# Performance work log

Hardware: AMD Instinct MI355X
Metric: run time of the kernel (lower is better)

The kernel has to match this reference:

```python
import jax, jax.numpy as jnp
import numpy as np

TEMPERATURE = 0.5  # NT-Xent temperature (SimCLR default in SACLR)
NEG_INF = -1e9


def ntxent(zi, zj, temperature=TEMPERATURE):
    """SimCLR NT-Xent between two views zi, zj of shape [B, D]."""
    B = zi.shape[0]
    z = jnp.concatenate([zi, zj], axis=0)                      # [2B, D]
    z = z / (jnp.linalg.norm(z, axis=1, keepdims=True) + 1e-8)  # cosine sim
    sim = (z @ z.T) / temperature                              # [2B, 2B]
    n = 2 * B
    sim = jnp.where(jnp.eye(n, dtype=bool), NEG_INF, sim)      # mask self
    labels = jnp.concatenate([jnp.arange(B) + B, jnp.arange(B)])
    logp = jax.nn.log_softmax(sim, axis=1)
    return -jnp.mean(logp[jnp.arange(n), labels])


def setup_inputs() -> dict:
    key = jax.random.key(0)
    k1, k2, k3 = jax.random.split(key, 3)
    B, D, W, H, CA = 512, 256, 14, 14, 8
    return {
        "global_feature": jax.random.normal(k1, (B, D), dtype=jnp.float32),
        "att": jax.random.uniform(k2, (B, CA, W, H), dtype=jnp.float32),
        "outputs": jax.random.normal(k3, (B, D, W, H), dtype=jnp.float32),
    }


def reference(global_feature, att, outputs):
    # attention = sum over attention-map channel, shape [B, W, H]
    attention = jnp.sum(att, axis=1)
    B, D, W, H = outputs.shape
    P = W * H
    # Flatten spatial positions in the same (i over W, j over H) row-major order
    # as the original nested python loops.
    local_feats = jnp.transpose(outputs, (2, 3, 0, 1)).reshape(P, B, D)   # [P, B, D]
    local_atts = jnp.transpose(attention, (1, 2, 0)).reshape(P, B)        # [P, B]

    # Faithful quirk of the original: global_feature is re-softmaxed at every
    # spatial position (it is reassigned inside the loop), so carry it in a scan.
    def step(g, xs):
        lf, la = xs
        g = jax.nn.softmax(g, axis=1)          # repeated softmax on global
        lf = jax.nn.softmax(lf, axis=1)        # softmax on local feature
        l = ntxent(lf, g) * jnp.mean(la) / P   # weighted NT-Xent term
        return g, l

    _, losses = jax.lax.scan(step, global_feature, (local_feats, local_atts))
    return jnp.sum(losses)
```

## Files before the change

### kernel.cpp

```cpp
#include <hip/hip_runtime.h>

#define B_   512
#define D_   256
#define P_   196
#define N2B  1024

typedef __attribute__((ext_vector_type(8))) short short8;
typedef __attribute__((ext_vector_type(4))) float f32x4;
typedef unsigned int u32;

#define LDSP(x) ((__attribute__((address_space(3))) u32*)(x))
#define GLBP(x) ((const __attribute__((address_space(1))) u32*)(x))

__device__ unsigned short g_Z[(size_t)P_ * N2B * D_];
__device__ float g_rowps[(size_t)P_ * 8 * N2B];
__device__ float g_pp2[P_ * 4];
__device__ float g_mApart[32 * P_];
__device__ float g_partials[P_];

static __device__ const unsigned char TROW36[36] = {
  0,0,0,0,0,0,0,0, 1,1,1,1,1,1,1, 2,2,2,2,2,2, 3,3,3,3,3, 4,4,4,4, 5,5,5, 6,6, 7};
static __device__ const unsigned char TCOL36[36] = {
  0,1,2,3,4,5,6,7, 1,2,3,4,5,6,7, 2,3,4,5,6,7, 3,4,5,6,7, 4,5,6,7, 5,6,7, 6,7, 7};

static __device__ inline unsigned short f2bf(float f) {
    union { float f; unsigned int u; } v; v.f = f;
    unsigned int u = v.u;
    return (unsigned short)((u + 0x7fffu + ((u >> 16) & 1u)) >> 16);
}
static __device__ inline float bf2f(unsigned short h) {
    union { unsigned int u; float f; } v; v.u = ((unsigned int)h) << 16;
    return v.f;
}
static __device__ inline float wave_sum(float v) {
    for (int off = 32; off > 0; off >>= 1) v += __shfl_xor(v, off, 64);
    return v;
}

__global__ __launch_bounds__(256) void gchain_kernel(const float* __restrict__ gf) {
    int wv = threadIdx.x >> 6, lane = threadIdx.x & 63;
    int b = blockIdx.x * 4 + wv;
    float4 g = ((const float4*)(gf + (size_t)b * D_))[lane];
    for (int p = 0; p < P_; ++p) {
        float e0 = __expf(g.x), e1 = __expf(g.y), e2 = __expf(g.z), e3 = __expf(g.w);
        float s1 = e0 + e1 + e2 + e3;
        float s2 = e0 * e0 + e1 * e1 + e2 * e2 + e3 * e3;
#pragma unroll
        for (int off = 32; off > 0; off >>= 1) {
            s1 += __shfl_xor(s1, off, 64);
            s2 += __shfl_xor(s2, off, 64);
        }
        float isq = rsqrtf(s2);
        ushort4 o;
        o.x = f2bf(e0 * isq); o.y = f2bf(e1 * isq); o.z = f2bf(e2 * isq); o.w = f2bf(e3 * isq);
        ((ushort4*)(g_Z + ((size_t)p * N2B + B_ + b) * D_))[lane] = o;
        float inv = 1.0f / s1;
        g.x = e0 * inv; g.y = e1 * inv; g.z = e2 * inv; g.w = e3 * inv;
    }
}

__global__ __launch_bounds__(1024) void lf_kernel(const float* __restrict__ outs) {
    __shared__ unsigned short vt[256 * 202];
    __shared__ float ss[256];
    int b = blockIdx.x, t = threadIdx.x;
    const float4* src4 = (const float4*)(outs + (size_t)b * (D_ * P_));
    for (int idx = t; idx < 12544; idx += 1024) {
        int d = idx / 49, c = idx - d * 49;
        float4 v = src4[idx];
        unsigned short* dst = vt + d * 202 + c * 4;
        ushort2 a, bb;
        a.x = f2bf(v.x); a.y = f2bf(v.y); bb.x = f2bf(v.z); bb.y = f2bf(v.w);
        *(ushort2*)dst = a; *(ushort2*)(dst + 2) = bb;
    }
    __syncthreads();
    {
        int p = t >> 2; if (p > 195) p = 195;
        int s = t & 3;
        float r = 0.0f;
        for (int dd = 0; dd < 64; ++dd) {
            float v = bf2f(vt[(s * 64 + dd) * 202 + p]);
            r += __expf(2.0f * v);
        }
        r += __shfl_xor(r, 1, 64);
        r += __shfl_xor(r, 2, 64);
        if (s == 0) ss[p] = rsqrtf(r);
    }
    __syncthreads();
    {
        int d = t & 255, q = t >> 8;
        for (int pi = 0; pi < 49; ++pi) {
            int p = q * 49 + pi;
            float v = bf2f(vt[d * 202 + p]);
            g_Z[((size_t)p * N2B + b) * D_ + d] = f2bf(__expf(v) * ss[p]);
        }
    }
}

__global__ __launch_bounds__(256) void meanA_kernel(const float* __restrict__ att) {
    int bk = blockIdx.x, t = threadIdx.x;
    if (t < P_) {
        float acc = 0.0f;
        const float* base = att + (size_t)bk * 128 * P_ + t;
        for (int r = 0; r < 128; ++r) acc += base[(size_t)r * P_];
        g_mApart[bk * P_ + t] = acc;
    }
}

__global__ __launch_bounds__(256, 3) void sim_kernel() {
    __shared__ __align__(16) unsigned short As[128 * 64];
    __shared__ __align__(16) unsigned short Bs[128 * 64];
    __shared__ float combuf[512];
    __shared__ float ppred[4];

    int lin0 = blockIdx.x;
    int xcd = lin0 & 7, slot = lin0 >> 3;
    int lin = xcd * 882 + slot;
    int p = lin / 36;
    int t36 = lin - p * 36;
    int trow = TROW36[t36], tcol = TCOL36[t36];

    int tid = threadIdx.x;
    int wv = tid >> 6, lane = tid & 63;
    int wr = wv >> 1, wc = wv & 1;
    int lr = lane & 15;
    int lk16 = (lane >> 4) * 16;

    const char* zb = (const char*)g_Z + (size_t)p * ((size_t)N2B * D_ * 2);
    const char* gA = zb + (size_t)trow * (128 * 512);
    const char* gB = zb + (size_t)tcol * (128 * 512);
    int lsub = (lane >> 3) * 512 + (lane & 7) * 16;

    f32x4 acc[4][4];
#pragma unroll
    for (int i = 0; i < 4; ++i)
#pragma unroll
        for (int j = 0; j < 4; ++j)
            acc[i][j] = (f32x4){0.0f, 0.0f, 0.0f, 0.0f};

    for (int ko = 0; ko < 4; ++ko) {
#pragma unroll
        for (int it = 0; it < 4; ++it) {
            int s = it * 4 + wv;
            int go = s * 4096 + ko * 128 + lsub;
            __builtin_amdgcn_global_load_lds(GLBP(gA + go), LDSP((char*)As + s * 1024), 16, 0, 0);
            __builtin_amdgcn_global_load_lds(GLBP(gB + go), LDSP((char*)Bs + s * 1024), 16, 0, 0);
        }
        __syncthreads();
#pragma unroll
        for (int ks = 0; ks < 2; ++ks) {
            short8 a[4], b[4];
#pragma unroll
            for (int i = 0; i < 4; ++i) {
                a[i] = *(const short8*)((const char*)As + (wr * 64 + i * 16 + lr) * 128 + ks * 64 + lk16);
                b[i] = *(const short8*)((const char*)Bs + (wc * 64 + i * 16 + lr) * 128 + ks * 64 + lk16);
            }
#pragma unroll
            for (int i = 0; i < 4; ++i)
#pragma unroll
                for (int j = 0; j < 4; ++j)
                    acc[i][j] = __builtin_amdgcn_mfma_f32_16x16x32_bf16(a[i], b[j], acc[i][j], 0, 0, 0);
        }
        __syncthreads();
    }

    bool DIAG = (trow == tcol);
    bool PART = (trow < 4) && (tcol == trow + 4);
    int r4 = (lane >> 4) * 4;
    float psum[4][4];
    float pcs[4] = {0.0f, 0.0f, 0.0f, 0.0f};
    float pp = 0.0f;
#pragma unroll
    for (int i = 0; i < 4; ++i)
#pragma unroll
        for (int r = 0; r < 4; ++r) psum[i][r] = 0.0f;

#pragma unroll
    for (int i = 0; i < 4; ++i) {
#pragma unroll
        for (int j = 0; j < 4; ++j) {
#pragma unroll
            for (int r = 0; r < 4; ++r) {
                float sv = 2.0f * acc[i][j][r];
                float e = __expf(sv);
                int lrow = wr * 64 + i * 16 + r4 + r;
                int lcol = wc * 64 + j * 16 + lr;
                bool ond = (lrow == lcol);
                if (DIAG && ond) e = 0.0f;
                psum[i][r] += e;
                pcs[j] += e;
                if (PART && ond) pp += sv;
            }
        }
    }

    float* rowbuf = combuf;
    float* colbuf = combuf + 256;
#pragma unroll
    for (int i = 0; i < 4; ++i)
#pragma unroll
        for (int r = 0; r < 4; ++r) {
            float ps = psum[i][r];
            ps += __shfl_xor(ps, 1, 64);
            ps += __shfl_xor(ps, 2, 64);
            ps += __shfl_xor(ps, 4, 64);
            ps += __shfl_xor(ps, 8, 64);
            if (lr == 0) rowbuf[wc * 128 + wr * 64 + i * 16 + r4 + r] = ps;
        }
#pragma unroll
    for (int j = 0; j < 4; ++j) {
        float pc = pcs[j];
        pc += __shfl_xor(pc, 16, 64);
        pc += __shfl_xor(pc, 32, 64);
        if (lane < 16) colbuf[wr * 128 + wc * 64 + j * 16 + lane] = pc;
    }
    float pw = PART ? wave_sum(pp) : 0.0f;
    if (lane == 0) ppred[wv] = pw;
    __syncthreads();

    if (tid < 128) {
        float v = rowbuf[tid] + rowbuf[128 + tid];
        g_rowps[((size_t)p * 8 + tcol) * N2B + trow * 128 + tid] = v;
    } else if (!DIAG) {
        int x = tid - 128;
        float v = colbuf[x] + colbuf[128 + x];
        g_rowps[((size_t)p * 8 + trow) * N2B + tcol * 128 + x] = v;
    }
    if (PART && tid == 0)
        g_pp2[p * 4 + trow] = 2.0f * (ppred[0] + ppred[1] + ppred[2] + ppred[3]);
}

__global__ __launch_bounds__(256) void rowreduce_kernel() {
    int p = blockIdx.x, t = threadIdx.x;
    const float* base = g_rowps + (size_t)p * 8 * N2B;
    float s = 0.0f;
    for (int r = t; r < N2B; r += 256) {
        float S = 0.0f;
#pragma unroll
        for (int k = 0; k < 8; ++k) S += base[(size_t)k * N2B + r];
        s += __logf(S);
    }
    s = wave_sum(s);
    __shared__ float red[4];
    int wv = t >> 6, lane = t & 63;
    if (lane == 0) red[wv] = s;
    __syncthreads();
    if (t == 0) {
        float tot = red[0] + red[1] + red[2] + red[3];
        float pp = g_pp2[p * 4 + 0] + g_pp2[p * 4 + 1] + g_pp2[p * 4 + 2] + g_pp2[p * 4 + 3];
        float ma = 0.0f;
        for (int k = 0; k < 32; ++k) ma += g_mApart[k * P_ + p];
        g_partials[p] = (tot - pp) * (ma * (1.0f / B_));
    }
}

__global__ __launch_bounds__(256) void final_kernel(float* __restrict__ out) {
    int t = threadIdx.x;
    float s = (t < P_) ? g_partials[t] : 0.0f;
    s = wave_sum(s);
    __shared__ float red[4];
    int wv = t >> 6, lane = t & 63;
    if (lane == 0) red[wv] = s;
    __syncthreads();
    if (t == 0) out[0] = (red[0] + red[1] + red[2] + red[3]) * (1.0f / ((float)N2B * (float)P_));
}

extern "C" void kernel_launch(void* const* d_in, const int* in_sizes, int n_in,
                              void* d_out, int out_size, void* d_ws, size_t ws_size,
                              hipStream_t stream) {
    const float* gf   = (const float*)d_in[0];
    const float* att  = (const float*)d_in[1];
    const float* outs = (const float*)d_in[2];
    float* out = (float*)d_out;

    hipLaunchKernelGGL(gchain_kernel, dim3(B_ / 4), dim3(256), 0, stream, gf);
    hipLaunchKernelGGL(lf_kernel, dim3(B_), dim3(1024), 0, stream, outs);
    hipLaunchKernelGGL(meanA_kernel, dim3(32), dim3(256), 0, stream, att);
    hipLaunchKernelGGL(sim_kernel, dim3(P_ * 36), dim3(256), 0, stream);
    hipLaunchKernelGGL(rowreduce_kernel, dim3(P_), dim3(256), 0, stream);
    hipLaunchKernelGGL(final_kernel, dim3(1), dim3(256), 0, stream, out);
}
```

Before: 372.6 us.

## Fuse prep kernels, pre-scale embeddings for exp2, swizzle LDS, specialize epilogue

Merges the global-chain, local-feature and attention-mean kernels into one heterogeneous prep launch, with the attention mean split over more slices. Folds the 1/temperature and log2(e) factors into the bf16 normalized embeddings so the epilogue can use exp2 directly. Adds an XOR swizzle to the LDS tile layout to reduce bank conflicts on the MFMA operand reads, and splits the epilogue into diagonal, positive-pair and plain variants so masking and column sums run only where needed. It also raises the launch-bounds occupancy hint. Scaling before bf16 rounding slightly changes numerics, and the fused prep kernel mixes 1024-thread blocks with very different per-block work.

```diff
diff --git a/kernel.cpp b/kernel.cpp
--- a/kernel.cpp
+++ b/kernel.cpp
@@ -5,6 +5,9 @@
 #define P_   196
 #define N2B  1024
 
+#define CSCALE 1.69864364f
+#define LN2    0.69314718f
+
 typedef __attribute__((ext_vector_type(8))) short short8;
 typedef __attribute__((ext_vector_type(4))) float f32x4;
 typedef unsigned int u32;
@@ -15,7 +18,7 @@
 __device__ unsigned short g_Z[(size_t)P_ * N2B * D_];
 __device__ float g_rowps[(size_t)P_ * 8 * N2B];
 __device__ float g_pp2[P_ * 4];
-__device__ float g_mApart[32 * P_];
+__device__ float g_mApart[128 * P_];
 __device__ float g_partials[P_];
 
 static __device__ const unsigned char TROW36[36] = {
@@ -37,76 +40,103 @@
     return v;
 }
 
-__global__ __launch_bounds__(256) void gchain_kernel(const float* __restrict__ gf) {
-    int wv = threadIdx.x >> 6, lane = threadIdx.x & 63;
-    int b = blockIdx.x * 4 + wv;
-    float4 g = ((const float4*)(gf + (size_t)b * D_))[lane];
-    for (int p = 0; p < P_; ++p) {
-        float e0 = __expf(g.x), e1 = __expf(g.y), e2 = __expf(g.z), e3 = __expf(g.w);
-        float s1 = e0 + e1 + e2 + e3;
-        float s2 = e0 * e0 + e1 * e1 + e2 * e2 + e3 * e3;
-#pragma unroll
-        for (int off = 32; off > 0; off >>= 1) {
-            s1 += __shfl_xor(s1, off, 64);
-            s2 += __shfl_xor(s2, off, 64);
-        }
-        float isq = rsqrtf(s2);
-        ushort4 o;
-        o.x = f2bf(e0 * isq); o.y = f2bf(e1 * isq); o.z = f2bf(e2 * isq); o.w = f2bf(e3 * isq);
-        ((ushort4*)(g_Z + ((size_t)p * N2B + B_ + b) * D_))[lane] = o;
-        float inv = 1.0f / s1;
-        g.x = e0 * inv; g.y = e1 * inv; g.z = e2 * inv; g.w = e3 * inv;
-    }
-}
-
-__global__ __launch_bounds__(1024) void lf_kernel(const float* __restrict__ outs) {
+__global__ __launch_bounds__(1024) void prep_kernel(const float* __restrict__ gf,
+                                                    const float* __restrict__ att,
+                                                    const float* __restrict__ outs) {
     __shared__ unsigned short vt[256 * 202];
     __shared__ float ss[256];
-    int b = blockIdx.x, t = threadIdx.x;
-    const float4* src4 = (const float4*)(outs + (size_t)b * (D_ * P_));
-    for (int idx = t; idx < 12544; idx += 1024) {
-        int d = idx / 49, c = idx - d * 49;
-        float4 v = src4[idx];
-        unsigned short* dst = vt + d * 202 + c * 4;
-        ushort2 a, bb;
-        a.x = f2bf(v.x); a.y = f2bf(v.y); bb.x = f2bf(v.z); bb.y = f2bf(v.w);
-        *(ushort2*)dst = a; *(ushort2*)(dst + 2) = bb;
-    }
-    __syncthreads();
-    {
-        int p = t >> 2; if (p > 195) p = 195;
-        int s = t & 3;
-        float r = 0.0f;
-        for (int dd = 0; dd < 64; ++dd) {
-            float v = bf2f(vt[(s * 64 + dd) * 202 + p]);
-            r += __expf(2.0f * v);
-        }
-        r += __shfl_xor(r, 1, 64);
-        r += __shfl_xor(r, 2, 64);
-        if (s == 0) ss[p] = rsqrtf(r);
-    }
-    __syncthreads();
-    {
-        int d = t & 255, q = t >> 8;
-        for (int pi = 0; pi < 49; ++pi) {
-            int p = q * 49 + pi;
-            float v = bf2f(vt[d * 202 + p]);
-            g_Z[((size_t)p * N2B + b) * D_ + d] = f2bf(__expf(v) * ss[p]);
-        }
-    }
-}
-
-__global__ __launch_bounds__(256) void meanA_kernel(const float* __restrict__ att) {
-    int bk = blockIdx.x, t = threadIdx.x;
-    if (t < P_) {
-        float acc = 0.0f;
-        const float* base = att + (size_t)bk * 128 * P_ + t;
-        for (int r = 0; r < 128; ++r) acc += base[(size_t)r * P_];
-        g_mApart[bk * P_ + t] = acc;
-    }
-}
-
-__global__ __launch_bounds__(256, 3) void sim_kernel() {
+    int blk = blockIdx.x, t = threadIdx.x;
+
+    if (blk < 32) {
+        int wv = t >> 6, lane = t & 63;
+        int b = blk * 16 + wv;
+        float4 g = ((const float4*)(gf + (size_t)b * D_))[lane];
+        for (int p = 0; p < P_; ++p) {
+            float e0 = __expf(g.x), e1 = __expf(g.y), e2 = __expf(g.z), e3 = __expf(g.w);
+            float s1 = e0 + e1 + e2 + e3;
+            float s2 = e0 * e0 + e1 * e1 + e2 * e2 + e3 * e3;
+#pragma unroll
+            for (int off = 32; off > 0; off >>= 1) {
+                s1 += __shfl_xor(s1, off, 64);
+                s2 += __shfl_xor(s2, off, 64);
+            }
+            float isq = rsqrtf(s2) * CSCALE;
+            ushort4 o;
+            o.x = f2bf(e0 * isq); o.y = f2bf(e1 * isq); o.z = f2bf(e2 * isq); o.w = f2bf(e3 * isq);
+            ((ushort4*)(g_Z + ((size_t)p * N2B + B_ + b) * D_))[lane] = o;
+            float inv = 1.0f / s1;
+            g.x = e0 * inv; g.y = e1 * inv; g.z = e2 * inv; g.w = e3 * inv;
+        }
+    } else if (blk < 64) {
+        int bk = blk - 32;
+        int sl = t >> 8, p = t & 255;
+        if (p < P_) {
+            float acc = 0.0f;
+            const float* base = att + ((size_t)bk * 128 + sl * 32) * P_ + p;
+            for (int r = 0; r < 32; ++r) acc += base[(size_t)r * P_];
+            g_mApart[(bk * 4 + sl) * P_ + p] = acc;
+        }
+    } else {
+        int b = blk - 64;
+        const float4* src4 = (const float4*)(outs + (size_t)b * (D_ * P_));
+        for (int idx = t; idx < 12544; idx += 1024) {
+            int d = idx / 49, c = idx - d * 49;
+            float4 v = src4[idx];
+            unsigned short* dst = vt + d * 202 + c * 4;
+            ushort2 a, bb;
+            a.x = f2bf(v.x); a.y = f2bf(v.y); bb.x = f2bf(v.z); bb.y = f2bf(v.w);
+            *(ushort2*)dst = a; *(ushort2*)(dst + 2) = bb;
+        }
+        __syncthreads();
+        {
+            int p = t >> 2; if (p > 195) p = 195;
+            int s = t & 3;
+            float r = 0.0f;
+            for (int dd = 0; dd < 64; ++dd) {
+                float v = bf2f(vt[(s * 64 + dd) * 202 + p]);
+                r += __expf(2.0f * v);
+            }
+            r += __shfl_xor(r, 1, 64);
+            r += __shfl_xor(r, 2, 64);
+            if (s == 0) ss[p] = rsqrtf(r) * CSCALE;
+        }
+        __syncthreads();
+        {
+            int d = t & 255, q = t >> 8;
+            for (int pi = 0; pi < 49; ++pi) {
+                int p = q * 49 + pi;
+                float v = bf2f(vt[d * 202 + p]);
+                g_Z[((size_t)p * N2B + b) * D_ + d] = f2bf(__expf(v) * ss[p]);
+            }
+        }
+    }
+}
+
+template<int MODE>
+static __device__ inline void do_epi(const f32x4 acc[4][4], float psum[4][4], float pcs[4],
+                                     float& pp, int wdiag, int lr, int r4) {
+#pragma unroll
+    for (int i = 0; i < 4; ++i) {
+#pragma unroll
+        for (int j = 0; j < 4; ++j) {
+#pragma unroll
+            for (int r = 0; r < 4; ++r) {
+                float a = acc[i][j][r];
+                float e = exp2f(a);
+                if (MODE == 1) {
+                    if (wdiag && i == j) e = (r4 + r == lr) ? 0.0f : e;
+                }
+                psum[i][r] += e;
+                if (MODE != 1) pcs[j] += e;
+                if (MODE == 2) {
+                    if (wdiag && i == j && (r4 + r == lr)) pp += a * LN2;
+                }
+            }
+        }
+    }
+}
+
+__global__ __launch_bounds__(256, 4) void sim_kernel() {
     __shared__ __align__(16) unsigned short As[128 * 64];
     __shared__ __align__(16) unsigned short Bs[128 * 64];
     __shared__ float combuf[512];
@@ -128,7 +158,7 @@
     const char* zb = (const char*)g_Z + (size_t)p * ((size_t)N2B * D_ * 2);
     const char* gA = zb + (size_t)trow * (128 * 512);
     const char* gB = zb + (size_t)tcol * (128 * 512);
-    int lsub = (lane >> 3) * 512 + (lane & 7) * 16;
+    int lsub = (lane >> 3) * 512 + (((lane & 7) ^ (lane >> 3)) << 4);
 
     f32x4 acc[4][4];
 #pragma unroll
@@ -148,11 +178,12 @@
         __syncthreads();
 #pragma unroll
         for (int ks = 0; ks < 2; ++ks) {
+            int kswz = (ks * 64 + lk16) ^ ((lr & 7) << 4);
             short8 a[4], b[4];
 #pragma unroll
             for (int i = 0; i < 4; ++i) {
-                a[i] = *(const short8*)((const char*)As + (wr * 64 + i * 16 + lr) * 128 + ks * 64 + lk16);
-                b[i] = *(const short8*)((const char*)Bs + (wc * 64 + i * 16 + lr) * 128 + ks * 64 + lk16);
+                a[i] = *(const short8*)((const char*)As + (wr * 64 + i * 16 + lr) * 128 + kswz);
+                b[i] = *(const short8*)((const char*)Bs + (wc * 64 + i * 16 + lr) * 128 + kswz);
             }
 #pragma unroll
             for (int i = 0; i < 4; ++i)
@@ -165,6 +196,7 @@
 
     bool DIAG = (trow == tcol);
     bool PART = (trow < 4) && (tcol == trow + 4);
+    int wdiag = (wr == wc);
     int r4 = (lane >> 4) * 4;
     float psum[4][4];
     float pcs[4] = {0.0f, 0.0f, 0.0f, 0.0f};
@@ -174,24 +206,9 @@
 #pragma unroll
         for (int r = 0; r < 4; ++r) psum[i][r] = 0.0f;
 
-#pragma unroll
-    for (int i = 0; i < 4; ++i) {
-#pragma unroll
-        for (int j = 0; j < 4; ++j) {
-#pragma unroll
-            for (int r = 0; r < 4; ++r) {
-                float sv = 2.0f * acc[i][j][r];
-                float e = __expf(sv);
-                int lrow = wr * 64 + i * 16 + r4 + r;
-                int lcol = wc * 64 + j * 16 + lr;
-                bool ond = (lrow == lcol);
-                if (DIAG && ond) e = 0.0f;
-                psum[i][r] += e;
-                pcs[j] += e;
-                if (PART && ond) pp += sv;
-            }
-        }
-    }
+    if (DIAG)      do_epi<1>(acc, psum, pcs, pp, wdiag, lr, r4);
+    else if (PART) do_epi<2>(acc, psum, pcs, pp, wdiag, lr, r4);
+    else           do_epi<0>(acc, psum, pcs, pp, wdiag, lr, r4);
 
     float* rowbuf = combuf;
     float* colbuf = combuf + 256;
@@ -206,15 +223,19 @@
             ps += __shfl_xor(ps, 8, 64);
             if (lr == 0) rowbuf[wc * 128 + wr * 64 + i * 16 + r4 + r] = ps;
         }
-#pragma unroll
-    for (int j = 0; j < 4; ++j) {
-        float pc = pcs[j];
-        pc += __shfl_xor(pc, 16, 64);
-        pc += __shfl_xor(pc, 32, 64);
-        if (lane < 16) colbuf[wr * 128 + wc * 64 + j * 16 + lane] = pc;
-    }
-    float pw = PART ? wave_sum(pp) : 0.0f;
-    if (lane == 0) ppred[wv] = pw;
+    if (!DIAG) {
+#pragma unroll
+        for (int j = 0; j < 4; ++j) {
+            float pc = pcs[j];
+            pc += __shfl_xor(pc, 16, 64);
+            pc += __shfl_xor(pc, 32, 64);
+            if (lane < 16) colbuf[wr * 128 + wc * 64 + j * 16 + lane] = pc;
+        }
+    }
+    if (PART) {
+        float pw = wave_sum(pp);
+        if (lane == 0) ppred[wv] = pw;
+    }
     __syncthreads();
 
     if (tid < 128) {
@@ -248,7 +269,7 @@
         float tot = red[0] + red[1] + red[2] + red[3];
         float pp = g_pp2[p * 4 + 0] + g_pp2[p * 4 + 1] + g_pp2[p * 4 + 2] + g_pp2[p * 4 + 3];
         float ma = 0.0f;
-        for (int k = 0; k < 32; ++k) ma += g_mApart[k * P_ + p];
+        for (int k = 0; k < 128; ++k) ma += g_mApart[k * P_ + p];
         g_partials[p] = (tot - pp) * (ma * (1.0f / B_));
     }
 }
@@ -272,9 +293,7 @@
     const float* outs = (const float*)d_in[2];
     float* out = (float*)d_out;
 
-    hipLaunchKernelGGL(gchain_kernel, dim3(B_ / 4), dim3(256), 0, stream, gf);
-    hipLaunchKernelGGL(lf_kernel, dim3(B_), dim3(1024), 0, stream, outs);
-    hipLaunchKernelGGL(meanA_kernel, dim3(32), dim3(256), 0, stream, att);
+    hipLaunchKernelGGL(prep_kernel, dim3(576), dim3(1024), 0, stream, gf, att, outs);
     hipLaunchKernelGGL(sim_kernel, dim3(P_ * 36), dim3(256), 0, stream);
     hipLaunchKernelGGL(rowreduce_kernel, dim3(P_), dim3(256), 0, stream);
     hipLaunchKernelGGL(final_kernel, dim3(1), dim3(256), 0, stream, out);
```

Measured after the change: 323.9 us. 13.1% less time.
